# Kernel optimization log

Measured on AMD Instinct MI355X. Metric: run time of the kernel, lower is better.

## Reference

```python
import jax, jax.numpy as jnp
import numpy as np

V_IN = 32000
V_OUT = 32000
E = 1024
H = 1024
B = 16
T = 512


def _lstm_layer(xs, Wih, Whh, bih, bhh):
    # xs: [T, B, in_dim]; PyTorch gate order: i, f, g, o (each size H)
    gx = jnp.einsum('tbi,gi->tbg', xs, Wih) + bih + bhh  # [T, B, 4H]

    def step(carry, g_t):
        h, c = carry
        g = g_t + h @ Whh.T  # [B, 4H]
        i, f, gg, o = jnp.split(g, 4, axis=-1)
        i = jax.nn.sigmoid(i)
        f = jax.nn.sigmoid(f)
        gg = jnp.tanh(gg)
        o = jax.nn.sigmoid(o)
        c = f * c + i * gg
        h = o * jnp.tanh(c)
        return (h, c), h

    h0 = jnp.zeros((xs.shape[1], Whh.shape[1]), dtype=xs.dtype)
    c0 = jnp.zeros_like(h0)
    _, hs = jax.lax.scan(step, (h0, c0), gx)
    return hs  # [T, B, H]


def setup_inputs() -> dict:
    key = jax.random.key(0)
    ks = jax.random.split(key, 12)
    s_e = 1.0  # nn.Embedding default init is N(0,1)
    s_l = 1.0 / np.sqrt(H)  # LSTM/Linear uniform bound 1/sqrt(H)

    def u(k, shape):
        return jax.random.uniform(k, shape, jnp.float32, -s_l, s_l)

    return {
        'x': jax.random.randint(ks[0], (B, T), 0, V_IN),
        'emb': jax.random.normal(ks[1], (V_IN, E), jnp.float32) * s_e,
        'W_ih0': u(ks[2], (4 * H, E)),
        'W_hh0': u(ks[3], (4 * H, H)),
        'b_ih0': u(ks[4], (4 * H,)),
        'b_hh0': u(ks[5], (4 * H,)),
        'W_ih1': u(ks[6], (4 * H, H)),
        'W_hh1': u(ks[7], (4 * H, H)),
        'b_ih1': u(ks[8], (4 * H,)),
        'b_hh1': u(ks[9], (4 * H,)),
        'W_out': u(ks[10], (V_OUT, H)),
        'b_out': u(ks[11], (V_OUT,)),
    }


def reference(x, emb, W_ih0, W_hh0, b_ih0, b_hh0, W_ih1, W_hh1, b_ih1, b_hh1, W_out, b_out):
    # embedding + permute to [T, B, E]
    out = emb[x].transpose(1, 0, 2)
    out = _lstm_layer(out, W_ih0, W_hh0, b_ih0, b_hh0)
    out = _lstm_layer(out, W_ih1, W_hh1, b_ih1, b_hh1)
    logits = jnp.einsum('tbh,oh->tbo', out, W_out) + b_out
    return logits.transpose(1, 0, 2)  # [B, T, V_OUT]
```

## Files before the change

### kernel.cpp

```cpp
#include <hip/hip_runtime.h>
#include <cstdint>
#include <cstddef>

typedef __bf16 bf16;
typedef float f32x4 __attribute__((ext_vector_type(4)));
typedef bf16 bf16x8 __attribute__((ext_vector_type(8)));
typedef bf16 bf16x4 __attribute__((ext_vector_type(4)));

#define AS1 __attribute__((address_space(1)))
#define AS3 __attribute__((address_space(3)))

__device__ __forceinline__ void gload_lds16(const void* g, void* l) {
  __builtin_amdgcn_global_load_lds((AS1 void*)g, (AS3 void*)l, 16, 0, 0);
}

#define NBLK_W 192
#define D0_WORDS (64 * 64)
#define D01_WORDS (128 * 64)
#define D1_WORDS (128 * 128)
#define FLAG_WORDS (D0_WORDS + D01_WORDS + D1_WORDS)

__global__ __launch_bounds__(256) void init_misc(
    const float* __restrict__ bih0, const float* __restrict__ bhh0,
    const float* __restrict__ bih1, const float* __restrict__ bhh1,
    float* __restrict__ bsum0, float* __restrict__ bsum1, unsigned* __restrict__ flags) {
  int i = blockIdx.x * 256 + threadIdx.x;
  if (i < 4096) {
    bsum0[i] = bih0[i] + bhh0[i];
    bsum1[i] = bih1[i] + bhh1[i];
  }
  for (int k = i; k < FLAG_WORDS; k += 64 * 256) flags[k] = 0u;
}

__global__ __launch_bounds__(256) void embed_gather(
    const int* __restrict__ x, const float* __restrict__ emb, bf16* __restrict__ xe, int T) {
  int row = blockIdx.x;
  int t = row >> 4, b = row & 15;
  int tok = x[b * T + t];
  int cix = threadIdx.x << 2;
  f32x4 v = *(const f32x4*)(emb + ((size_t)tok << 10) + cix);
  bf16x4 o;
  for (int j = 0; j < 4; ++j) o[j] = (bf16)v[j];
  *(bf16x4*)(xe + ((size_t)row << 10) + cix) = o;
}

template <int OUTMODE>
__global__ __launch_bounds__(256) void gemm_bf16(
    const bf16* __restrict__ A, const float* __restrict__ Bw,
    const float* __restrict__ bias, float* __restrict__ C,
    int M, int N, int K, int Tdim) {
  __shared__ bf16 aL[2][128 * 32];
  __shared__ bf16 bL[2][128 * 32];
  const int tid = threadIdx.x;
  const int l = tid & 63, w = tid >> 6;
  const int nbm = M >> 7;
  const int bm = blockIdx.x % nbm;
  const int bn = blockIdx.x / nbm;
  const int wr = (w >> 1) << 6, wc = (w & 1) << 6;
  const int NT = K >> 5;
  const int r16 = l & 15, kq = l >> 4;

  f32x4 acc[4][4];
  for (int m = 0; m < 4; ++m)
    for (int n = 0; n < 4; ++n) acc[m][n] = (f32x4){0.f, 0.f, 0.f, 0.f};

  for (int i = 0; i < 2; ++i) {
    int lin = tid + (i << 8);
    int r = lin >> 2, s = lin & 3, c = s ^ (r & 3);
    gload_lds16(A + (size_t)((bm << 7) + r) * K + (c << 3), &aL[0][lin << 3]);
  }
  for (int i = 0; i < 2; ++i) {
    int lin = tid + (i << 8);
    int r = lin >> 2, c = lin & 3;
    const float* src = Bw + (size_t)((bn << 7) + r) * K + (c << 3);
    f32x4 v0 = *(const f32x4*)src;
    f32x4 v1 = *(const f32x4*)(src + 4);
    bf16x8 o;
    for (int j = 0; j < 4; ++j) { o[j] = (bf16)v0[j]; o[j + 4] = (bf16)v1[j]; }
    *(bf16x8*)&bL[0][(r << 5) + ((c ^ (r & 3)) << 3)] = o;
  }
  __syncthreads();

  for (int kt = 0; kt < NT; ++kt) {
    const int cur = kt & 1;
    const bool pf = (kt + 1 < NT);
    f32x4 bv0[2], bv1[2];
    int br_[2], bs_[2];
    if (pf) {
      for (int i = 0; i < 2; ++i) {
        int lin = tid + (i << 8);
        int r = lin >> 2, s = lin & 3, c = s ^ (r & 3);
        gload_lds16(A + (size_t)((bm << 7) + r) * K + ((kt + 1) << 5) + (c << 3),
                    &aL[cur ^ 1][lin << 3]);
      }
      for (int i = 0; i < 2; ++i) {
        int lin = tid + (i << 8);
        int r = lin >> 2, c = lin & 3;
        const float* src = Bw + (size_t)((bn << 7) + r) * K + ((kt + 1) << 5) + (c << 3);
        bv0[i] = *(const f32x4*)src;
        bv1[i] = *(const f32x4*)(src + 4);
        br_[i] = r;
        bs_[i] = c ^ (r & 3);
      }
    }
    bf16x8 af[4], bfr[4];
    for (int m = 0; m < 4; ++m) {
      int row = wr + (m << 4) + r16;
      int ch = kq ^ (row & 3);
      af[m] = *(const bf16x8*)&aL[cur][(row << 5) + (ch << 3)];
    }
    for (int n = 0; n < 4; ++n) {
      int row = wc + (n << 4) + r16;
      int ch = kq ^ (row & 3);
      bfr[n] = *(const bf16x8*)&bL[cur][(row << 5) + (ch << 3)];
    }
    for (int m = 0; m < 4; ++m)
      for (int n = 0; n < 4; ++n)
        acc[m][n] = __builtin_amdgcn_mfma_f32_16x16x32_bf16(af[m], bfr[n], acc[m][n], 0, 0, 0);
    if (pf) {
      for (int i = 0; i < 2; ++i) {
        bf16x8 o;
        for (int j = 0; j < 4; ++j) { o[j] = (bf16)bv0[i][j]; o[j + 4] = (bf16)bv1[i][j]; }
        *(bf16x8*)&bL[cur ^ 1][(br_[i] << 5) + (bs_[i] << 3)] = o;
      }
    }
    __syncthreads();
  }

  float bvv[4];
  for (int n = 0; n < 4; ++n) bvv[n] = bias[(bn << 7) + wc + (n << 4) + r16];
  for (int m = 0; m < 4; ++m) {
    int Rbase = (bm << 7) + wr + (m << 4) + (kq << 2);
    for (int r = 0; r < 4; ++r) {
      int R = Rbase + r;
      size_t rowoff;
      if (OUTMODE == 0) {
        rowoff = (size_t)R * N;
      } else {
        int tt = R >> 4, bb = R & 15;
        rowoff = ((size_t)bb * Tdim + tt) * N;
      }
      for (int n = 0; n < 4; ++n)
        C[rowoff + (bn << 7) + wc + (n << 4) + r16] = acc[m][n][r] + bvv[n];
    }
  }
}

__global__ __launch_bounds__(256, 1) void lstm_pipe(
    const float* __restrict__ gx,
    const float* __restrict__ Whh0,
    const float* __restrict__ Wih1,
    const float* __restrict__ Whh1,
    const float* __restrict__ bsum1,
    bf16* __restrict__ hs0,
    bf16* __restrict__ hs1,
    unsigned* __restrict__ flags,
    int T) {
  __shared__ bf16 wlds[64 * 1024];
  __shared__ float glds[4 * 16 * 16];
  const int tid = threadIdx.x;
  const int l = tid & 63, w = tid >> 6;
  const int bid = blockIdx.x;
  unsigned* const done0 = flags;
  unsigned* const done01 = flags + D0_WORDS;
  unsigned* const done1 = flags + D0_WORDS + D01_WORDS;

  const bool L0 = bid < 64;
  const int r16 = l & 15, kq = l >> 4, rx = r16 & 7;

  if (L0) {
    const int j0s = bid << 4;
    for (int it = 0; it < 32; ++it) {
      int lin = tid + (it << 8);
      int row = lin >> 7, cs = lin & 127, c = cs ^ (row & 7);
      int g = row >> 4, n = row & 15;
      const float* src = Whh0 + (size_t)(g * 1024 + j0s + n) * 1024 + (c << 3);
      f32x4 v0 = *(const f32x4*)src;
      f32x4 v1 = *(const f32x4*)(src + 4);
      bf16x8 o;
      for (int j = 0; j < 4; ++j) { o[j] = (bf16)v0[j]; o[j + 4] = (bf16)v1[j]; }
      *(bf16x8*)(wlds + (row << 10) + (cs << 3)) = o;
    }
  } else {
    const int j0s = (bid - 64) << 3;
    for (int it = 0; it < 32; ++it) {
      int lin = tid + (it << 8);
      int row = lin >> 7, cs = lin & 127, c = cs ^ (row & 7);
      int m = row >> 5, rr = row & 31, g = rr >> 3, n = rr & 7;
      const float* W = m ? Whh1 : Wih1;
      const float* src = W + (size_t)(g * 1024 + j0s + n) * 1024 + (c << 3);
      f32x4 v0 = *(const f32x4*)src;
      f32x4 v1 = *(const f32x4*)(src + 4);
      bf16x8 o;
      for (int j = 0; j < 4; ++j) { o[j] = (bf16)v0[j]; o[j + 4] = (bf16)v1[j]; }
      *(bf16x8*)(wlds + (row << 10) + (cs << 3)) = o;
    }
  }
  __syncthreads();

  if (L0) {
    const int j0 = bid << 4;
    const int bidx = tid >> 4, jl = tid & 15;
    float cst = 0.f;

    for (int t = 0; t < T; ++t) {
      const float* gp = gx + ((((size_t)t << 4) + bidx) << 12) + j0 + jl;
      float gi = gp[0], gf = gp[1024], gg2 = gp[2048], go_ = gp[3072];
      if (t > 0 && w == 0) {
        const unsigned* fp = done0 + (bid << 6) + l;
        while (__hip_atomic_load(fp, __ATOMIC_RELAXED, __HIP_MEMORY_SCOPE_AGENT) <
               (unsigned)t) {
        }
      }
      __syncthreads();
      asm volatile("" ::: "memory");

      f32x4 acc = (f32x4){0.f, 0.f, 0.f, 0.f};
      f32x4 acc2 = (f32x4){0.f, 0.f, 0.f, 0.f};
      if (t > 0) {
        const bf16* hp = hs0 + ((size_t)(t - 1) << 14) + (r16 << 10) + (kq << 3);
        const bf16* wb = wlds + (((w << 4) + r16) << 10);
#pragma unroll 8
        for (int kk = 0; kk < 32; kk += 2) {
          bf16x8 a0 = *(const bf16x8*)(hp + (kk << 5));
          bf16x8 a1 = *(const bf16x8*)(hp + ((kk + 1) << 5));
          acc = __builtin_amdgcn_mfma_f32_16x16x32_bf16(
              a0, *(const bf16x8*)(wb + ((((kk << 2) + kq) ^ rx) << 3)), acc, 0, 0, 0);
          acc2 = __builtin_amdgcn_mfma_f32_16x16x32_bf16(
              a1, *(const bf16x8*)(wb + (((((kk + 1) << 2) + kq) ^ rx) << 3)), acc2, 0, 0, 0);
        }
      }
      for (int r = 0; r < 4; ++r)
        glds[(w << 8) + (((kq << 2) + r) << 4) + r16] = acc[r] + acc2[r];
      __syncthreads();

      float xi = glds[(bidx << 4) + jl] + gi;
      float xf = glds[256 + (bidx << 4) + jl] + gf;
      float xg = glds[512 + (bidx << 4) + jl] + gg2;
      float xo = glds[768 + (bidx << 4) + jl] + go_;
      float ig = 1.f / (1.f + __expf(-xi));
      float fg = 1.f / (1.f + __expf(-xf));
      float eg = __expf(2.f * xg);
      float ggv = 1.f - 2.f / (eg + 1.f);
      float og = 1.f / (1.f + __expf(-xo));
      cst = fg * cst + ig * ggv;
      float ec = __expf(2.f * cst);
      float th = 1.f - 2.f / (ec + 1.f);
      bf16 hb = (bf16)(og * th);
      unsigned hu = (unsigned)__builtin_bit_cast(unsigned short, hb);
      unsigned other = (unsigned)__shfl_xor((int)hu, 1, 64);
      if (!(tid & 1)) {
        unsigned pair = (hu & 0xffffu) | (other << 16);
        bf16* sp = hs0 + ((((size_t)t << 4) + bidx) << 10) + j0 + jl;
        asm volatile("global_store_dword %0, %1, off sc1" ::"v"(sp), "v"(pair) : "memory");
      }
      asm volatile("s_waitcnt vmcnt(0)" ::: "memory");
      __syncthreads();

      const unsigned ep = (unsigned)(t + 1);
      if (w == 0)
        __hip_atomic_store(done0 + (l << 6) + bid, ep, __ATOMIC_RELAXED,
                           __HIP_MEMORY_SCOPE_AGENT);
      else if (w == 1)
        __hip_atomic_store(done01 + (l << 6) + bid, ep, __ATOMIC_RELAXED,
                           __HIP_MEMORY_SCOPE_AGENT);
      else if (w == 2)
        __hip_atomic_store(done01 + ((64 + l) << 6) + bid, ep, __ATOMIC_RELAXED,
                           __HIP_MEMORY_SCOPE_AGENT);
    }
  } else {
    const int q = bid - 64;
    const int j0 = q << 3;
    const int b1 = tid >> 3, j1 = tid & 7;
    float cst = 0.f;
    float bi_ = 0.f, bf_ = 0.f, bg_ = 0.f, bo_ = 0.f;
    if (tid < 128) {
      bi_ = bsum1[j0 + j1];
      bf_ = bsum1[1024 + j0 + j1];
      bg_ = bsum1[2048 + j0 + j1];
      bo_ = bsum1[3072 + j0 + j1];
    }

    for (int t1 = 0; t1 < T; ++t1) {
      if (w == 0) {
        const unsigned* fp = done01 + (q << 6) + l;
        while (__hip_atomic_load(fp, __ATOMIC_RELAXED, __HIP_MEMORY_SCOPE_AGENT) <
               (unsigned)(t1 + 1)) {
        }
      } else if (w == 1 && t1 > 0) {
        const unsigned* fp = done1 + (q << 7) + l;
        while (__hip_atomic_load(fp, __ATOMIC_RELAXED, __HIP_MEMORY_SCOPE_AGENT) <
               (unsigned)t1) {
        }
      } else if (w == 2 && t1 > 0) {
        const unsigned* fp = done1 + (q << 7) + 64 + l;
        while (__hip_atomic_load(fp, __ATOMIC_RELAXED, __HIP_MEMORY_SCOPE_AGENT) <
               (unsigned)t1) {
        }
      }
      __syncthreads();
      asm volatile("" ::: "memory");

      f32x4 acc0 = (f32x4){0.f, 0.f, 0.f, 0.f};
      f32x4 acc1 = (f32x4){0.f, 0.f, 0.f, 0.f};
      const bf16* hp0 = hs0 + ((size_t)t1 << 14) + (r16 << 10) + (kq << 3);
      const bf16* wb0 = wlds + (((w << 3) + rx) << 10);
      const bf16* wb1 = wlds + ((32 + (w << 3) + rx) << 10);
#pragma unroll 8
      for (int kk = 0; kk < 32; ++kk) {
        bf16x8 a0 = *(const bf16x8*)(hp0 + (kk << 5));
        acc0 = __builtin_amdgcn_mfma_f32_16x16x32_bf16(
            a0, *(const bf16x8*)(wb0 + ((((kk << 2) + kq) ^ rx) << 3)), acc0, 0, 0, 0);
      }
      if (t1 > 0) {
        const bf16* hp1 = hs1 + ((size_t)(t1 - 1) << 14) + (r16 << 10) + (kq << 3);
#pragma unroll 8
        for (int kk = 0; kk < 32; ++kk) {
          bf16x8 a1 = *(const bf16x8*)(hp1 + (kk << 5));
          acc1 = __builtin_amdgcn_mfma_f32_16x16x32_bf16(
              a1, *(const bf16x8*)(wb1 + ((((kk << 2) + kq) ^ rx) << 3)), acc1, 0, 0, 0);
        }
      }
      for (int r = 0; r < 4; ++r)
        glds[(w << 8) + (((kq << 2) + r) << 4) + r16] = acc0[r] + acc1[r];
      __syncthreads();

      if (tid < 128) {
        float xi = glds[(b1 << 4) + j1] + bi_;
        float xf = glds[256 + (b1 << 4) + j1] + bf_;
        float xg = glds[512 + (b1 << 4) + j1] + bg_;
        float xo = glds[768 + (b1 << 4) + j1] + bo_;
        float ig = 1.f / (1.f + __expf(-xi));
        float fg = 1.f / (1.f + __expf(-xf));
        float eg = __expf(2.f * xg);
        float ggv = 1.f - 2.f / (eg + 1.f);
        float og = 1.f / (1.f + __expf(-xo));
        cst = fg * cst + ig * ggv;
        float ec = __expf(2.f * cst);
        float th = 1.f - 2.f / (ec + 1.f);
        bf16 hb = (bf16)(og * th);
        unsigned hu = (unsigned)__builtin_bit_cast(unsigned short, hb);
        unsigned other = (unsigned)__shfl_xor((int)hu, 1, 64);
        if (!(tid & 1)) {
          unsigned pair = (hu & 0xffffu) | (other << 16);
          bf16* sp = hs1 + ((((size_t)t1 << 4) + b1) << 10) + j0 + j1;
          asm volatile("global_store_dword %0, %1, off sc1" ::"v"(sp), "v"(pair) : "memory");
        }
      }
      asm volatile("s_waitcnt vmcnt(0)" ::: "memory");
      __syncthreads();

      const unsigned ep = (unsigned)(t1 + 1);
      if (w == 0)
        __hip_atomic_store(done1 + (l << 7) + q, ep, __ATOMIC_RELAXED,
                           __HIP_MEMORY_SCOPE_AGENT);
      else if (w == 1)
        __hip_atomic_store(done1 + ((64 + l) << 7) + q, ep, __ATOMIC_RELAXED,
                           __HIP_MEMORY_SCOPE_AGENT);
    }
  }
}

extern "C" void kernel_launch(void* const* d_in, const int* in_sizes, int n_in,
                              void* d_out, int out_size, void* d_ws, size_t ws_size,
                              hipStream_t stream) {
  const int* x = (const int*)d_in[0];
  const float* emb = (const float*)d_in[1];
  const float* Wih0 = (const float*)d_in[2];
  const float* Whh0 = (const float*)d_in[3];
  const float* bih0 = (const float*)d_in[4];
  const float* bhh0 = (const float*)d_in[5];
  const float* Wih1 = (const float*)d_in[6];
  const float* Whh1 = (const float*)d_in[7];
  const float* bih1 = (const float*)d_in[8];
  const float* bhh1 = (const float*)d_in[9];
  const float* Wout = (const float*)d_in[10];
  const float* bout = (const float*)d_in[11];

  const int T = 512, H = 1024, V = 32000;
  const int M = T * 16;
  const size_t bfb = (size_t)M * H * 2;

  char* p = (char*)d_ws;
  bf16* hs1 = (bf16*)p;           p += bfb;
  float* bsum0 = (float*)p;       p += 4096 * 4;
  float* bsum1 = (float*)p;       p += 4096 * 4;
  unsigned* flags = (unsigned*)p; p += FLAG_WORDS * 4;
  size_t base_need = (size_t)(p - (char*)d_ws);
  bf16 *xe, *hs0;
  if (ws_size >= base_need + 2 * bfb) {
    xe = (bf16*)p;
    hs0 = (bf16*)(p + bfb);
  } else {
    char* tail = (char*)d_out + (size_t)out_size * 4 - 2 * bfb;
    xe = (bf16*)tail;
    hs0 = (bf16*)(tail + bfb);
  }
  float* gx = (float*)d_out;

  init_misc<<<64, 256, 0, stream>>>(bih0, bhh0, bih1, bhh1, bsum0, bsum1, flags);
  embed_gather<<<M, 256, 0, stream>>>(x, emb, xe, T);
  gemm_bf16<0><<<(M / 128) * (4096 / 128), 256, 0, stream>>>(xe, Wih0, bsum0, gx, M, 4096, H, 0);
  lstm_pipe<<<NBLK_W, 256, 0, stream>>>(gx, Whh0, Wih1, Whh1, bsum1, hs0, hs1, flags, T);
  gemm_bf16<1><<<(M / 128) * (V / 128), 256, 0, stream>>>(hs1, Wout, bout, (float*)d_out, M, V, H, T);
}
```

Before: 5.997 ms.

## Replace per-reader replicated flag arrays with a single shared flag per block

```diff
diff --git a/kernel.cpp b/kernel.cpp
--- a/kernel.cpp
+++ b/kernel.cpp
@@ -15,10 +15,7 @@
 }
 
 #define NBLK_W 192
-#define D0_WORDS (64 * 64)
-#define D01_WORDS (128 * 64)
-#define D1_WORDS (128 * 128)
-#define FLAG_WORDS (D0_WORDS + D01_WORDS + D1_WORDS)
+#define FLAG_WORDS 256
 
 __global__ __launch_bounds__(256) void init_misc(
     const float* __restrict__ bih0, const float* __restrict__ bhh0,
@@ -29,7 +26,7 @@
     bsum0[i] = bih0[i] + bhh0[i];
     bsum1[i] = bih1[i] + bhh1[i];
   }
-  for (int k = i; k < FLAG_WORDS; k += 64 * 256) flags[k] = 0u;
+  if (i < FLAG_WORDS) flags[i] = 0u;
 }
 
 __global__ __launch_bounds__(256) void embed_gather(
@@ -161,9 +158,8 @@
   const int tid = threadIdx.x;
   const int l = tid & 63, w = tid >> 6;
   const int bid = blockIdx.x;
-  unsigned* const done0 = flags;
-  unsigned* const done01 = flags + D0_WORDS;
-  unsigned* const done1 = flags + D0_WORDS + D01_WORDS;
+  unsigned* const flag0 = flags;
+  unsigned* const flag1 = flags + 64;
 
   const bool L0 = bid < 64;
   const int r16 = l & 15, kq = l >> 4, rx = r16 & 7;
@@ -207,7 +203,7 @@
       const float* gp = gx + ((((size_t)t << 4) + bidx) << 12) + j0 + jl;
       float gi = gp[0], gf = gp[1024], gg2 = gp[2048], go_ = gp[3072];
       if (t > 0 && w == 0) {
-        const unsigned* fp = done0 + (bid << 6) + l;
+        const unsigned* fp = flag0 + l;
         while (__hip_atomic_load(fp, __ATOMIC_RELAXED, __HIP_MEMORY_SCOPE_AGENT) <
                (unsigned)t) {
         }
@@ -257,15 +253,8 @@
       asm volatile("s_waitcnt vmcnt(0)" ::: "memory");
       __syncthreads();
 
-      const unsigned ep = (unsigned)(t + 1);
-      if (w == 0)
-        __hip_atomic_store(done0 + (l << 6) + bid, ep, __ATOMIC_RELAXED,
-                           __HIP_MEMORY_SCOPE_AGENT);
-      else if (w == 1)
-        __hip_atomic_store(done01 + (l << 6) + bid, ep, __ATOMIC_RELAXED,
-                           __HIP_MEMORY_SCOPE_AGENT);
-      else if (w == 2)
-        __hip_atomic_store(done01 + ((64 + l) << 6) + bid, ep, __ATOMIC_RELAXED,
+      if (tid == 0)
+        __hip_atomic_store(flag0 + bid, (unsigned)(t + 1), __ATOMIC_RELAXED,
                            __HIP_MEMORY_SCOPE_AGENT);
     }
   } else {
@@ -283,17 +272,17 @@
 
     for (int t1 = 0; t1 < T; ++t1) {
       if (w == 0) {
-        const unsigned* fp = done01 + (q << 6) + l;
+        const unsigned* fp = flag0 + l;
         while (__hip_atomic_load(fp, __ATOMIC_RELAXED, __HIP_MEMORY_SCOPE_AGENT) <
                (unsigned)(t1 + 1)) {
         }
       } else if (w == 1 && t1 > 0) {
-        const unsigned* fp = done1 + (q << 7) + l;
+        const unsigned* fp = flag1 + l;
         while (__hip_atomic_load(fp, __ATOMIC_RELAXED, __HIP_MEMORY_SCOPE_AGENT) <
                (unsigned)t1) {
         }
       } else if (w == 2 && t1 > 0) {
-        const unsigned* fp = done1 + (q << 7) + 64 + l;
+        const unsigned* fp = flag1 + 64 + l;
         while (__hip_atomic_load(fp, __ATOMIC_RELAXED, __HIP_MEMORY_SCOPE_AGENT) <
                (unsigned)t1) {
         }
@@ -350,12 +339,8 @@
       asm volatile("s_waitcnt vmcnt(0)" ::: "memory");
       __syncthreads();
 
-      const unsigned ep = (unsigned)(t1 + 1);
-      if (w == 0)
-        __hip_atomic_store(done1 + (l << 7) + q, ep, __ATOMIC_RELAXED,
-                           __HIP_MEMORY_SCOPE_AGENT);
-      else if (w == 1)
-        __hip_atomic_store(done1 + ((64 + l) << 7) + q, ep, __ATOMIC_RELAXED,
+      if (tid == 0)
+        __hip_atomic_store(flag1 + q, (unsigned)(t1 + 1), __ATOMIC_RELAXED,
                            __HIP_MEMORY_SCOPE_AGENT);
     }
   }
```

Measured after the change: 6.613 ms. +10.3%, slower.
